# Kernel tuning notes

Hardware: AMD Instinct MI355X
Metric: run time of the kernel (lower is better)

## Reference

```python
import jax, jax.numpy as jnp
import numpy as np
from jax import lax

H = 51  # hidden size hardcoded in SequenceLSTM


def setup_inputs() -> dict:
    key = jax.random.key(0)
    ks = jax.random.split(key, 12)
    B, T = 256, 2048
    init = lambda k, sh: jax.random.normal(k, sh, dtype=jnp.float32) * 0.08
    return {
        "x": jax.random.normal(ks[0], (B, T), dtype=jnp.float32),
        "W_ih1": init(ks[1], (4 * H, 1)),
        "W_hh1": init(ks[2], (4 * H, H)),
        "b_ih1": init(ks[3], (4 * H,)),
        "b_hh1": init(ks[4], (4 * H,)),
        "W_ih2": init(ks[5], (4 * H, H)),
        "W_hh2": init(ks[6], (4 * H, H)),
        "b_ih2": init(ks[7], (4 * H,)),
        "b_hh2": init(ks[8], (4 * H,)),
        "fc_w": init(ks[9], (1, H)),
        "fc_b": init(ks[10], (1,)),
        "future": 64,
    }


def _cell(xt, h, c, Wih, Whh, bih, bhh):
    # PyTorch LSTMCell: gates in order i, f, g, o
    g = xt @ Wih.T + h @ Whh.T + (bih + bhh)
    i, f, gg, o = jnp.split(g, 4, axis=-1)
    c = jax.nn.sigmoid(f) * c + jax.nn.sigmoid(i) * jnp.tanh(gg)
    h = jax.nn.sigmoid(o) * jnp.tanh(c)
    return h, c


def reference(x, W_ih1, W_hh1, b_ih1, b_hh1, W_ih2, W_hh2, b_ih2, b_hh2,
              fc_w, fc_b, future):
    B = x.shape[0]
    z = jnp.zeros((B, H), dtype=x.dtype)

    def step(carry, xt):  # xt: [B, 1]
        h1, c1, h2, c2 = carry
        h1, c1 = _cell(xt, h1, c1, W_ih1, W_hh1, b_ih1, b_hh1)
        h2, c2 = _cell(h1, h2, c2, W_ih2, W_hh2, b_ih2, b_hh2)
        out = h2 @ fc_w.T + fc_b  # [B, 1]
        return (h1, c1, h2, c2), out

    carry, outs = lax.scan(step, (z, z, z, z), x.T[:, :, None])  # outs: [T, B, 1]

    if future > 0:
        def fstep(carry, _):
            h1, c1, h2, c2, out = carry
            h1, c1 = _cell(out, h1, c1, W_ih1, W_hh1, b_ih1, b_hh1)
            h2, c2 = _cell(h1, h2, c2, W_ih2, W_hh2, b_ih2, b_hh2)
            out = h2 @ fc_w.T + fc_b
            return (h1, c1, h2, c2, out), out

        fcarry = (*carry, outs[-1])
        _, fouts = lax.scan(fstep, fcarry, None, length=future)
        outs = jnp.concatenate([outs, fouts], axis=0)

    return outs[:, :, 0].T  # [B, T + future]
```

## Files before the change

kernel.cpp:

```cpp
#include <hip/hip_runtime.h>

#define H 51

__device__ __forceinline__ float rl_(float v, int lane) {
    return __builtin_bit_cast(float, __builtin_amdgcn_readlane(__builtin_bit_cast(int, v), lane));
}
template<int CTRL>
__device__ __forceinline__ float qb_(float v) {
    return __builtin_bit_cast(float, __builtin_amdgcn_update_dpp(
        0, __builtin_bit_cast(int, v), CTRL, 0xf, 0xf, true));
}

__device__ __forceinline__ float act_(float x, float m2, float A, float B) {
    const float e = __builtin_amdgcn_exp2f(m2 * x);
    const float r = __builtin_amdgcn_rcpf(1.f + e);
    return fmaf(A, r, B);
}
__device__ __forceinline__ float tanh_(float c) {
    const float e = __builtin_amdgcn_exp2f(2.885390082f * c);
    const float r = __builtin_amdgcn_rcpf(1.f + e);
    return fmaf(-2.f, r, 1.f);
}

#define FOR51(M) \
 M(0) M(1) M(2) M(3) M(4) M(5) M(6) M(7) M(8) M(9) \
 M(10) M(11) M(12) M(13) M(14) M(15) M(16) M(17) M(18) M(19) \
 M(20) M(21) M(22) M(23) M(24) M(25) M(26) M(27) M(28) M(29) \
 M(30) M(31) M(32) M(33) M(34) M(35) M(36) M(37) M(38) M(39) \
 M(40) M(41) M(42) M(43) M(44) M(45) M(46) M(47) M(48) M(49) M(50)

#define FOR51_RR(M) \
 M(0,0) M(1,1) M(2,2) M(3,3) M(4,0) M(5,1) M(6,2) M(7,3) \
 M(8,0) M(9,1) M(10,2) M(11,3) M(12,0) M(13,1) M(14,2) M(15,3) \
 M(16,0) M(17,1) M(18,2) M(19,3) M(20,0) M(21,1) M(22,2) M(23,3) \
 M(24,0) M(25,1) M(26,2) M(27,3) M(28,0) M(29,1) M(30,2) M(31,3) \
 M(32,0) M(33,1) M(34,2) M(35,3) M(36,0) M(37,1) M(38,2) M(39,3) \
 M(40,0) M(41,1) M(42,2) M(43,3) M(44,0) M(45,1) M(46,2) M(47,3) \
 M(48,0) M(49,1) M(50,2)

__global__ __launch_bounds__(768)
__attribute__((amdgpu_waves_per_eu(3, 3)))
void lstm_seq_kernel(const float* __restrict__ x,
                     const float* __restrict__ Wih1, const float* __restrict__ Whh1,
                     const float* __restrict__ bih1, const float* __restrict__ bhh1,
                     const float* __restrict__ Wih2, const float* __restrict__ Whh2,
                     const float* __restrict__ bih2, const float* __restrict__ bhh2,
                     const float* __restrict__ fcw, const float* __restrict__ fcb,
                     float* __restrict__ out, int T, int future)
{
    const int b   = blockIdx.x;
    const int tid = threadIdx.x;
    const int l   = tid & 63;
    const int w   = tid >> 6;
    const int grp = w >> 2;
    const int j   = w & 3;
    const int uq  = l >> 2;
    const int g   = l & 3;
    const int u   = 13 * j + uq;
    const bool act_lane = (uq < 13) && (u < H);
    const bool g0lane   = act_lane && (g == 0);
    const int row = act_lane ? (g * H + u) : 0;

    extern __shared__ float xld[];
    __shared__ float h1s[2][64];
    __shared__ float h2s[2][64];
    __shared__ float hh2buf[220];
    __shared__ __align__(16) float fcp[4];

    for (int i = tid; i < T; i += 768) xld[i] = x[(size_t)b * T + i];
    if (tid < 64) { h1s[0][tid] = 0.f; h1s[1][tid] = 0.f;
                    h2s[0][tid] = 0.f; h2s[1][tid] = 0.f; }
    if (tid < 4) fcp[tid] = 0.f;

    const float* Wm = (grp == 0) ? Whh1 : ((grp == 1) ? Whh2 : Wih2);
    const size_t rb = (size_t)row * H;
    #define DECLW(k) float wt_##k;
    FOR51(DECLW)
    #define LOADW(k) wt_##k = Wm[rb + k];
    FOR51(LOADW)
    #define PINW(k) asm volatile("" : "+v"(wt_##k));
    FOR51(PINW)

    const float wx1   = (grp == 0 && act_lane) ? Wih1[row] : 0.f;
    const float bias1 = (grp == 0 && act_lane) ? (bih1[row] + bhh1[row]) : 0.f;
    const float bias2 = (grp == 2 && act_lane) ? (bih2[row] + bhh2[row]) : 0.f;
    const float fcu   = (grp == 2 && g0lane) ? fcw[u] : 0.f;
    const float fcb_l = fcb[0];

    const float m2A = (g == 2) ? 2.885390082f : -1.442695041f;
    const float Aa  = act_lane ? ((g == 2) ? -2.f : 1.f) : 0.f;
    const float Ba  = (act_lane && g == 2) ? 1.f : 0.f;

    float cc = 0.f;
    __syncthreads();

    const int TT = T + future;
    for (int t = 0; t < TT; ++t) {
        const int p = t & 1, q = p ^ 1;

        float o = 0.f;
        if (t > 0) {
            const float4 f = *(const float4*)fcp;
            o = (f.x + f.y) + (f.z + f.w) + fcb_l;
            if (tid == 0) out[(size_t)b * TT + (t - 1)] = o;
        }

        if (grp == 0) {
            const float xt = (t < T) ? xld[t] : o;
            const float hv = h1s[q][l];
            float a0 = 0.f, a1 = 0.f, a2 = 0.f, a3 = 0.f;
            #define MACB(k, jj) a##jj = fmaf(rl_(hv, k), wt_##k, a##jj);
            FOR51_RR(MACB)
            const float pre1 = bias1 + fmaf(wx1, xt, (a0 + a1) + (a2 + a3));
            const float a = act_(pre1, m2A, Aa, Ba);
            const float si = qb_<0x00>(a);
            const float sf = qb_<0x55>(a);
            const float tg = qb_<0xAA>(a);
            const float so = qb_<0xFF>(a);
            cc = fmaf(sf, cc, si * tg);
            const float h1n = so * tanh_(cc);
            if (g0lane) h1s[p][u] = h1n;
        } else if (grp == 1) {
            const float hv = h2s[q][l];
            float a0 = 0.f, a1 = 0.f, a2 = 0.f, a3 = 0.f;
            FOR51_RR(MACB)
            if (act_lane) hh2buf[52 * j + l] = (a0 + a1) + (a2 + a3);
        }
        __syncthreads();

        if (grp == 2) {
            const float hv = h1s[p][l];
            float a0 = 0.f, a1 = 0.f, a2 = 0.f, a3 = 0.f;
            FOR51_RR(MACB)
            const float hh2 = act_lane ? hh2buf[52 * j + l] : 0.f;
            const float pre2 = bias2 + hh2 + ((a0 + a1) + (a2 + a3));
            const float a = act_(pre2, m2A, Aa, Ba);
            const float si = qb_<0x00>(a);
            const float sf = qb_<0x55>(a);
            const float tg = qb_<0xAA>(a);
            const float so = qb_<0xFF>(a);
            cc = fmaf(sf, cc, si * tg);
            const float h2n = so * tanh_(cc);
            if (g0lane) h2s[p][u] = h2n;

            float pv = g0lane ? h2n * fcu : 0.f;
            pv += __shfl_xor(pv, 4, 64);
            pv += __shfl_xor(pv, 8, 64);
            pv += __shfl_xor(pv, 16, 64);
            pv += __shfl_xor(pv, 32, 64);
            if (l == 0) fcp[j] = pv;
        }
        __syncthreads();
    }

    if (tid == 0) {
        const float4 f = *(const float4*)fcp;
        out[(size_t)b * TT + (TT - 1)] = (f.x + f.y) + (f.z + f.w) + fcb_l;
    }
}

extern "C" void kernel_launch(void* const* d_in, const int* in_sizes, int n_in,
                              void* d_out, int out_size, void* d_ws, size_t ws_size,
                              hipStream_t stream) {
    const float* x    = (const float*)d_in[0];
    const float* Wih1 = (const float*)d_in[1];
    const float* Whh1 = (const float*)d_in[2];
    const float* bih1 = (const float*)d_in[3];
    const float* bhh1 = (const float*)d_in[4];
    const float* Wih2 = (const float*)d_in[5];
    const float* Whh2 = (const float*)d_in[6];
    const float* bih2 = (const float*)d_in[7];
    const float* bhh2 = (const float*)d_in[8];
    const float* fcw  = (const float*)d_in[9];
    const float* fcb  = (const float*)d_in[10];
    float* out = (float*)d_out;

    const int B  = 256;
    const int T  = in_sizes[0] / B;
    const int TT = out_size / B;
    const int future = TT - T;

    const size_t shmem = (size_t)T * sizeof(float);
    hipLaunchKernelGGL(lstm_seq_kernel, dim3(B), dim3(768), shmem, stream,
                       x, Wih1, Whh1, bih1, bhh1, Wih2, Whh2, bih2, bhh2,
                       fcw, fcb, out, T, future);
}
```

Baseline: 2.438 ms.

## Split LSTM weights between registers and LDS to cut VGPR pressure

Only the first 32 weight columns per row stay in registers; the remaining 19 (padded to 20) are staged in LDS and read as five float4 loads per step. The x sequence is no longer staged in LDS but prefetched from global memory one step ahead, and the fixed waves-per-EU attribute is dropped. This lowers register use, possibly allowing more resident blocks, at the cost of extra LDS reads inside the serial recurrence and roughly 49KB of static LDS per block.

```diff
diff --git a/kernel.cpp b/kernel.cpp
--- a/kernel.cpp
+++ b/kernel.cpp
@@ -1,6 +1,9 @@
 #include <hip/hip_runtime.h>
 
 #define H 51
+#define NROW 612
+#define WREG 32
+#define WSTR 20
 
 __device__ __forceinline__ float rl_(float v, int lane) {
     return __builtin_bit_cast(float, __builtin_amdgcn_readlane(__builtin_bit_cast(int, v), lane));
@@ -22,24 +25,18 @@
     return fmaf(-2.f, r, 1.f);
 }
 
-#define FOR51(M) \
+#define FOR32(M) \
  M(0) M(1) M(2) M(3) M(4) M(5) M(6) M(7) M(8) M(9) \
  M(10) M(11) M(12) M(13) M(14) M(15) M(16) M(17) M(18) M(19) \
- M(20) M(21) M(22) M(23) M(24) M(25) M(26) M(27) M(28) M(29) \
- M(30) M(31) M(32) M(33) M(34) M(35) M(36) M(37) M(38) M(39) \
- M(40) M(41) M(42) M(43) M(44) M(45) M(46) M(47) M(48) M(49) M(50)
-
-#define FOR51_RR(M) \
+ M(20) M(21) M(22) M(23) M(24) M(25) M(26) M(27) M(28) M(29) M(30) M(31)
+
+#define FOR32_RR(M) \
  M(0,0) M(1,1) M(2,2) M(3,3) M(4,0) M(5,1) M(6,2) M(7,3) \
  M(8,0) M(9,1) M(10,2) M(11,3) M(12,0) M(13,1) M(14,2) M(15,3) \
  M(16,0) M(17,1) M(18,2) M(19,3) M(20,0) M(21,1) M(22,2) M(23,3) \
- M(24,0) M(25,1) M(26,2) M(27,3) M(28,0) M(29,1) M(30,2) M(31,3) \
- M(32,0) M(33,1) M(34,2) M(35,3) M(36,0) M(37,1) M(38,2) M(39,3) \
- M(40,0) M(41,1) M(42,2) M(43,3) M(44,0) M(45,1) M(46,2) M(47,3) \
- M(48,0) M(49,1) M(50,2)
+ M(24,0) M(25,1) M(26,2) M(27,3) M(28,0) M(29,1) M(30,2) M(31,3)
 
 __global__ __launch_bounds__(768)
-__attribute__((amdgpu_waves_per_eu(3, 3)))
 void lstm_seq_kernel(const float* __restrict__ x,
                      const float* __restrict__ Wih1, const float* __restrict__ Whh1,
                      const float* __restrict__ bih1, const float* __restrict__ bhh1,
@@ -61,25 +58,34 @@
     const bool g0lane   = act_lane && (g == 0);
     const int row = act_lane ? (g * H + u) : 0;
 
-    extern __shared__ float xld[];
+    __shared__ __align__(16) float wlds[NROW * WSTR];
     __shared__ float h1s[2][64];
     __shared__ float h2s[2][64];
     __shared__ float hh2buf[220];
     __shared__ __align__(16) float fcp[4];
 
-    for (int i = tid; i < T; i += 768) xld[i] = x[(size_t)b * T + i];
+    for (int i = tid; i < NROW * WSTR; i += 768) {
+        const int r  = i / WSTR;
+        const int kk = i % WSTR;
+        float v = 0.f;
+        if (kk < WSTR - 1) {
+            const int m  = r / 204;
+            const int rr = r % 204;
+            const float* W = (m == 0) ? Whh1 : ((m == 1) ? Whh2 : Wih2);
+            v = W[rr * H + WREG + kk];
+        }
+        wlds[i] = v;
+    }
     if (tid < 64) { h1s[0][tid] = 0.f; h1s[1][tid] = 0.f;
                     h2s[0][tid] = 0.f; h2s[1][tid] = 0.f; }
     if (tid < 4) fcp[tid] = 0.f;
 
     const float* Wm = (grp == 0) ? Whh1 : ((grp == 1) ? Whh2 : Wih2);
-    const size_t rb = (size_t)row * H;
-    #define DECLW(k) float wt_##k;
-    FOR51(DECLW)
-    #define LOADW(k) wt_##k = Wm[rb + k];
-    FOR51(LOADW)
-    #define PINW(k) asm volatile("" : "+v"(wt_##k));
-    FOR51(PINW)
+    const int rb = row * H;
+    #define DECLW(k) float wt_##k = Wm[rb + k];
+    FOR32(DECLW)
+
+    const float* wrow = &wlds[(grp * 204 + row) * WSTR];
 
     const float wx1   = (grp == 0 && act_lane) ? Wih1[row] : 0.f;
     const float bias1 = (grp == 0 && act_lane) ? (bih1[row] + bhh1[row]) : 0.f;
@@ -92,7 +98,20 @@
     const float Ba  = (act_lane && g == 2) ? 1.f : 0.f;
 
     float cc = 0.f;
+    float xt_pre = (grp == 0) ? x[(size_t)b * T] : 0.f;
+
     __syncthreads();
+
+    #define MR(k, jj) a##jj = fmaf(rl_(hv, k), wt_##k, a##jj);
+    #define MAC4(Q, KB) \
+        a0 = fmaf(rl_(hv, KB + 0), Q.x, a0); \
+        a1 = fmaf(rl_(hv, KB + 1), Q.y, a1); \
+        a2 = fmaf(rl_(hv, KB + 2), Q.z, a2); \
+        a3 = fmaf(rl_(hv, KB + 3), Q.w, a3);
+    #define DOT_TAIL() \
+        const float4* wf = (const float4*)wrow; \
+        const float4 q0 = wf[0], q1 = wf[1], q2 = wf[2], q3 = wf[3], q4 = wf[4]; \
+        MAC4(q0, 32) MAC4(q1, 36) MAC4(q2, 40) MAC4(q3, 44) MAC4(q4, 48)
 
     const int TT = T + future;
     for (int t = 0; t < TT; ++t) {
@@ -106,11 +125,12 @@
         }
 
         if (grp == 0) {
-            const float xt = (t < T) ? xld[t] : o;
+            const float xt = (t < T) ? xt_pre : o;
+            if (t + 1 < T) xt_pre = x[(size_t)b * T + t + 1];
             const float hv = h1s[q][l];
             float a0 = 0.f, a1 = 0.f, a2 = 0.f, a3 = 0.f;
-            #define MACB(k, jj) a##jj = fmaf(rl_(hv, k), wt_##k, a##jj);
-            FOR51_RR(MACB)
+            FOR32_RR(MR)
+            DOT_TAIL()
             const float pre1 = bias1 + fmaf(wx1, xt, (a0 + a1) + (a2 + a3));
             const float a = act_(pre1, m2A, Aa, Ba);
             const float si = qb_<0x00>(a);
@@ -123,7 +143,8 @@
         } else if (grp == 1) {
             const float hv = h2s[q][l];
             float a0 = 0.f, a1 = 0.f, a2 = 0.f, a3 = 0.f;
-            FOR51_RR(MACB)
+            FOR32_RR(MR)
+            DOT_TAIL()
             if (act_lane) hh2buf[52 * j + l] = (a0 + a1) + (a2 + a3);
         }
         __syncthreads();
@@ -131,7 +152,8 @@
         if (grp == 2) {
             const float hv = h1s[p][l];
             float a0 = 0.f, a1 = 0.f, a2 = 0.f, a3 = 0.f;
-            FOR51_RR(MACB)
+            FOR32_RR(MR)
+            DOT_TAIL()
             const float hh2 = act_lane ? hh2buf[52 * j + l] : 0.f;
             const float pre2 = bias2 + hh2 + ((a0 + a1) + (a2 + a3));
             const float a = act_(pre2, m2A, Aa, Ba);
@@ -180,8 +202,7 @@
     const int TT = out_size / B;
     const int future = TT - T;
 
-    const size_t shmem = (size_t)T * sizeof(float);
-    hipLaunchKernelGGL(lstm_seq_kernel, dim3(B), dim3(768), shmem, stream,
+    hipLaunchKernelGGL(lstm_seq_kernel, dim3(B), dim3(768), 0, stream,
                        x, Wih1, Whh1, bih1, bhh1, Wih2, Whh2, bih2, bhh2,
                        fcw, fcb, out, T, future);
 }
```

Result: slower. 2.522 ms (+3.4%).
